# Performance work log

Measured on AMD Instinct MI355X. Metric: run time of the kernel, lower is better.

The kernel has to match this reference:

```python
import jax, jax.numpy as jnp
import numpy as np

N_NODES = 100000
N_EDGES = 1200000
IN_DIM = 256
HID = 64


def _spmm(rows, cols, vals, M):
    # sparse (COO) @ dense: gather source rows, scale by edge vals, scatter-add to dest
    gathered = M[cols] * vals[:, None]          # [E, d]
    return jax.ops.segment_sum(gathered, rows, num_segments=N_NODES)


def _gcn_embed(rows, cols, vals, X, W1, b1, W2, b2):
    # layer 1: SELU(A @ (X W1) + b1)
    Z = _spmm(rows, cols, vals, X @ W1) + b1
    Z = jax.nn.selu(Z)
    # layer 2: A @ (Z W2) + b2 (no activation)
    Z = _spmm(rows, cols, vals, Z @ W2) + b2
    # row-wise L2 normalize (F.normalize, p=2, dim=1)
    norm = jnp.sqrt(jnp.sum(Z * Z, axis=1, keepdims=True))
    return Z / jnp.maximum(norm, 1e-12)


def setup_inputs() -> dict:
    key = jax.random.key(0)
    ks = jax.random.split(key, 10)
    X1 = jax.random.normal(ks[0], (N_NODES, IN_DIM), dtype=jnp.float32)
    X2 = jax.random.normal(ks[1], (N_NODES, IN_DIM), dtype=jnp.float32)
    rows1 = jax.random.randint(ks[2], (N_EDGES,), 0, N_NODES, dtype=jnp.int32)
    cols1 = jax.random.randint(ks[3], (N_EDGES,), 0, N_NODES, dtype=jnp.int32)
    vals1 = jax.random.uniform(ks[4], (N_EDGES,), dtype=jnp.float32)
    rows2 = jax.random.randint(ks[5], (N_EDGES,), 0, N_NODES, dtype=jnp.int32)
    cols2 = jax.random.randint(ks[6], (N_EDGES,), 0, N_NODES, dtype=jnp.int32)
    vals2 = jax.random.uniform(ks[7], (N_EDGES,), dtype=jnp.float32)
    # Xavier-uniform weights, zero biases (reset_parameters)
    lim1 = float(np.sqrt(6.0 / (IN_DIM + HID)))
    lim2 = float(np.sqrt(6.0 / (HID + HID)))
    W1 = jax.random.uniform(ks[8], (IN_DIM, HID), dtype=jnp.float32, minval=-lim1, maxval=lim1)
    W2 = jax.random.uniform(ks[9], (HID, HID), dtype=jnp.float32, minval=-lim2, maxval=lim2)
    b1 = jnp.zeros((HID,), dtype=jnp.float32)
    b2 = jnp.zeros((HID,), dtype=jnp.float32)
    return {"X1": X1, "X2": X2, "rows1": rows1, "cols1": cols1, "vals1": vals1,
            "rows2": rows2, "cols2": cols2, "vals2": vals2,
            "W1": W1, "b1": b1, "W2": W2, "b2": b2}


def reference(X1, X2, rows1, cols1, vals1, rows2, cols2, vals2, W1, b1, W2, b2):
    Z1 = _gcn_embed(rows1, cols1, vals1, X1, W1, b1, W2, b2)
    Z2 = _gcn_embed(rows2, cols2, vals2, X2, W1, b1, W2, b2)
    return (Z1, Z2)
```

## Files before the change

### kernel.cpp

```cpp
#include <hip/hip_runtime.h>
#include <hip/hip_bf16.h>


#define RPB 512
#define EPB 4096
#define MAXB 8192

typedef __attribute__((ext_vector_type(8))) short short8;
typedef __attribute__((ext_vector_type(4))) short short4v;
typedef __attribute__((ext_vector_type(4))) float f32x4;

#define GEMM_LDS 36864
#define SCAT_LDS 52224
#define SORT_LDS 72704

__device__ __forceinline__ float selu_f(float x) {
    const float scale = 1.0507009873554805f;
    const float alpha = 1.6732632423543772f;
    return x > 0.0f ? scale * x : scale * alpha * (__expf(x) - 1.0f);
}

__device__ __forceinline__ short f2bf(float x) {
    unsigned u = __float_as_uint(x);
    u += 0x7FFF + ((u >> 16) & 1);
    return (short)(u >> 16);
}
__device__ __forceinline__ float bf2f(short h) {
    return __uint_as_float(((unsigned)(unsigned short)h) << 16);
}

__global__ void scan_a(const int* __restrict__ countsB, int* __restrict__ offsB,
                       int* __restrict__ partialsB, int N) {
    const int* counts = countsB + (size_t)blockIdx.y * N;
    int* offs = offsB + (size_t)blockIdx.y * (N + 1);
    int* partials = partialsB + (size_t)blockIdx.y * 512;
    __shared__ int sh[256];
    int tid = threadIdx.x;
    int base = blockIdx.x * 1024 + tid * 4;
    int4 c = make_int4(0, 0, 0, 0);
    if (base + 3 < N) {
        c = *(const int4*)(counts + base);
    } else {
        if (base + 0 < N) c.x = counts[base + 0];
        if (base + 1 < N) c.y = counts[base + 1];
        if (base + 2 < N) c.z = counts[base + 2];
        if (base + 3 < N) c.w = counts[base + 3];
    }
    int tsum = c.x + c.y + c.z + c.w;
    sh[tid] = tsum;
    __syncthreads();
    int val = tsum;
    for (int d = 1; d < 256; d <<= 1) {
        int t = (tid >= d) ? sh[tid - d] : 0;
        __syncthreads();
        val += t;
        sh[tid] = val;
        __syncthreads();
    }
    int excl = val - tsum;
    int4 o;
    o.x = excl; o.y = o.x + c.x; o.z = o.y + c.y; o.w = o.z + c.z;
    if (base + 3 < N) {
        *(int4*)(offs + base) = o;
    } else {
        if (base + 0 < N) offs[base + 0] = o.x;
        if (base + 1 < N) offs[base + 1] = o.y;
        if (base + 2 < N) offs[base + 2] = o.z;
        if (base + 3 < N) offs[base + 3] = o.w;
    }
    if (tid == 255) partials[blockIdx.x] = val;
}

__global__ void scan_b(int* __restrict__ partialsB, int nb) {
    int* partials = partialsB + (size_t)blockIdx.y * 512;
    __shared__ int sh[128];
    int tid = threadIdx.x;
    int v = (tid < nb) ? partials[tid] : 0;
    sh[tid] = v;
    __syncthreads();
    int val = v;
    for (int d = 1; d < 128; d <<= 1) {
        int t = (tid >= d) ? sh[tid - d] : 0;
        __syncthreads();
        val += t;
        sh[tid] = val;
        __syncthreads();
    }
    if (tid < nb) partials[tid] = val - v;
}

__global__ void scan_c(int* __restrict__ offsB, const int* __restrict__ partialsB,
                       int N, int E) {
    int* offs = offsB + (size_t)blockIdx.y * (N + 1);
    const int* partials = partialsB + (size_t)blockIdx.y * 512;
    int tid = threadIdx.x;
    int base = blockIdx.x * 1024 + tid * 4;
    int add = partials[blockIdx.x];
    if (base + 3 < N) {
        int4 o = *(int4*)(offs + base);
        o.x += add; o.y += add; o.z += add; o.w += add;
        *(int4*)(offs + base) = o;
    } else {
        for (int t = 0; t < 4; t++)
            if (base + t < N) offs[base + t] += add;
    }
    if (blockIdx.x == 0 && tid == 0) offs[N] = E;
}


__device__ __forceinline__ void role_hist(const int* __restrict__ rows,
                                          int* __restrict__ cntT,
                                          int E, int nbA, int NB, int bx,
                                          int* cnt) {
    int tid = threadIdx.x;
    cnt[tid] = 0;
    __syncthreads();
    int e0 = bx * EPB;
#pragma unroll
    for (int k = 0; k < EPB / 256; k++) {
        int e = e0 + k * 256 + tid;
        if (e < E) atomicAdd(&cnt[rows[e] >> 9], 1);
    }
    __syncthreads();
    if (tid < NB) cntT[tid * nbA + bx] = cnt[tid];
}

__device__ __forceinline__ void role_scatter(const int* __restrict__ rows,
                                             const int* __restrict__ cols,
                                             const float* __restrict__ vals,
                                             const int* __restrict__ csOffs,
                                             int2* __restrict__ ecvA,
                                             int E, int nbA, int NB, int bx,
                                             char* smem) {
    int* cnt = (int*)smem;
    int* loc = cnt + 256;
    int* gof = loc + 256;
    int* dstBase = gof + 256;
    int2* eLDS = (int2*)(dstBase + EPB);
    int tid = threadIdx.x;
    int e0 = bx * EPB;
    cnt[tid] = 0;
    __syncthreads();
#pragma unroll
    for (int k = 0; k < EPB / 256; k++) {
        int e = e0 + k * 256 + tid;
        if (e < E) atomicAdd(&cnt[rows[e] >> 9], 1);
    }
    __syncthreads();
    int my = cnt[tid];
    loc[tid] = my;
    __syncthreads();
    int val = my;
    for (int d = 1; d < 256; d <<= 1) {
        int t = (tid >= d) ? loc[tid - d] : 0;
        __syncthreads();
        val += t;
        loc[tid] = val;
        __syncthreads();
    }
    int excl = val - my;
    loc[tid] = excl;
    cnt[tid] = excl;
    gof[tid] = (tid < NB) ? csOffs[tid * nbA + bx] : 0;
    __syncthreads();
#pragma unroll
    for (int k = 0; k < EPB / 256; k++) {
        int e = e0 + k * 256 + tid;
        if (e < E) {
            int r = rows[e];
            int b = r >> 9;
            int p = atomicAdd(&cnt[b], 1);
            eLDS[p] = make_int2(((r & (RPB - 1)) << 17) | cols[e],
                                __float_as_int(vals[e]));
            dstBase[p] = gof[b] - loc[b];
        }
    }
    __syncthreads();
    int nE = min(EPB, E - e0);
    for (int j = tid; j < nE; j += 256)
        ecvA[dstBase[j] + j] = eLDS[j];
}

__device__ __forceinline__ void role_sort(const int* __restrict__ csOffs,
                                          const int2* __restrict__ ecvA,
                                          int2* __restrict__ ecv,
                                          int* __restrict__ offs,
                                          int nbA, int N, int E, int b,
                                          char* smem) {
    int* rcnt = (int*)smem;
    int* roff = rcnt + 512;
    int* rcur = roff + 512;
    int* sh   = rcur + 512;
    int2* eLDS = (int2*)(sh + 256);
    int tid = threadIdx.x;
    int bs = csOffs[b * nbA];
    int be = csOffs[(b + 1) * nbA];
    int cntE = be - bs;
    if (cntE > MAXB) cntE = MAXB;
    rcnt[tid] = 0;
    rcnt[tid + 256] = 0;
    __syncthreads();
    for (int j = tid; j < cntE; j += 256)
        atomicAdd(&rcnt[ecvA[bs + j].x >> 17], 1);
    __syncthreads();
    int a0 = rcnt[2 * tid], a1 = rcnt[2 * tid + 1];
    int ps = a0 + a1;
    sh[tid] = ps;
    __syncthreads();
    int val = ps;
    for (int d = 1; d < 256; d <<= 1) {
        int t = (tid >= d) ? sh[tid - d] : 0;
        __syncthreads();
        val += t;
        sh[tid] = val;
        __syncthreads();
    }
    int exclPair = val - ps;
    roff[2 * tid] = exclPair;
    roff[2 * tid + 1] = exclPair + a0;
    rcur[2 * tid] = exclPair;
    rcur[2 * tid + 1] = exclPair + a0;
    __syncthreads();
    int row0 = b * RPB;
    for (int t2 = tid; t2 < RPB; t2 += 256) {
        int row = row0 + t2;
        if (row <= N) offs[row] = bs + roff[t2];
    }
    if (b == 0 && tid == 0) offs[N] = E;
    for (int j = tid; j < cntE; j += 256) {
        int2 p = ecvA[bs + j];
        int pos = atomicAdd(&rcur[p.x >> 17], 1);
        if (pos < MAXB) eLDS[pos] = make_int2(p.x & 0x1FFFF, p.y);
    }
    __syncthreads();
    for (int j = tid; j < cntE; j += 256)
        ecv[bs + j] = eLDS[j];
}

__device__ __forceinline__ void role_gemm256(const float* __restrict__ A,
                                             const short* __restrict__ Wth,
                                             const short* __restrict__ Wtl,
                                             float* __restrict__ C, int M,
                                             int tile, char* smem) {
    constexpr int K = 256, NC = K / 64;
    short* Ah = (short*)smem;
    short* Al = Ah + 64 * 72;
    short* Wh = Al + 64 * 72;
    short* Wl = Wh + 64 * 72;
    int tid = threadIdx.x;
    int wave = tid >> 6, lane = tid & 63;
    int m = lane & 15, q = lane >> 4;
    int row0 = tile * 64;
    int ai = tid >> 4;
    int aj = (tid & 15) * 4;
    f32x4 acc[4] = {{0.f, 0.f, 0.f, 0.f}, {0.f, 0.f, 0.f, 0.f},
                    {0.f, 0.f, 0.f, 0.f}, {0.f, 0.f, 0.f, 0.f}};
    float4 ga[4];
#pragma unroll
    for (int v = 0; v < 4; v++) {
        int gr = row0 + v * 16 + ai;
        ga[v] = make_float4(0.f, 0.f, 0.f, 0.f);
        if (gr < M) ga[v] = *(const float4*)(A + (size_t)gr * K + aj);
    }
#pragma unroll
    for (int c = 0; c < NC; c++) {
        short4v whv[4], wlv[4];
#pragma unroll
        for (int v = 0; v < 4; v++) {
            size_t wo = (size_t)(v * 16 + ai) * K + c * 64 + aj;
            whv[v] = *(const short4v*)(Wth + wo);
            wlv[v] = *(const short4v*)(Wtl + wo);
        }
        float4 gan[4];
        if (c + 1 < NC) {
#pragma unroll
            for (int v = 0; v < 4; v++) {
                int gr = row0 + v * 16 + ai;
                gan[v] = make_float4(0.f, 0.f, 0.f, 0.f);
                if (gr < M)
                    gan[v] = *(const float4*)(A + (size_t)gr * K + (c + 1) * 64 + aj);
            }
        }
#pragma unroll
        for (int v = 0; v < 4; v++) {
            int r = v * 16 + ai;
            float f[4] = {ga[v].x, ga[v].y, ga[v].z, ga[v].w};
            short4v h, l;
#pragma unroll
            for (int j = 0; j < 4; j++) {
                short hh = f2bf(f[j]);
                h[j] = hh;
                l[j] = f2bf(f[j] - bf2f(hh));
            }
            *(short4v*)(&Ah[r * 72 + aj]) = h;
            *(short4v*)(&Al[r * 72 + aj]) = l;
        }
#pragma unroll
        for (int v = 0; v < 4; v++) {
            int n = v * 16 + ai;
            *(short4v*)(&Wh[n * 72 + aj]) = whv[v];
            *(short4v*)(&Wl[n * 72 + aj]) = wlv[v];
        }
        __syncthreads();
        int ar = (16 * wave + m) * 72;
        short8 ah0 = *(const short8*)(&Ah[ar + q * 8]);
        short8 ah1 = *(const short8*)(&Ah[ar + 32 + q * 8]);
        short8 al0 = *(const short8*)(&Al[ar + q * 8]);
        short8 al1 = *(const short8*)(&Al[ar + 32 + q * 8]);
#pragma unroll
        for (int nt = 0; nt < 4; nt++) {
            int nb = (nt * 16 + m) * 72;
            short8 bh0 = *(const short8*)(&Wh[nb + q * 8]);
            short8 bh1 = *(const short8*)(&Wh[nb + 32 + q * 8]);
            short8 bl0 = *(const short8*)(&Wl[nb + q * 8]);
            short8 bl1 = *(const short8*)(&Wl[nb + 32 + q * 8]);
            acc[nt] = __builtin_amdgcn_mfma_f32_16x16x32_bf16(ah0, bh0, acc[nt], 0, 0, 0);
            acc[nt] = __builtin_amdgcn_mfma_f32_16x16x32_bf16(al0, bh0, acc[nt], 0, 0, 0);
            acc[nt] = __builtin_amdgcn_mfma_f32_16x16x32_bf16(ah0, bl0, acc[nt], 0, 0, 0);
            acc[nt] = __builtin_amdgcn_mfma_f32_16x16x32_bf16(ah1, bh1, acc[nt], 0, 0, 0);
            acc[nt] = __builtin_amdgcn_mfma_f32_16x16x32_bf16(al1, bh1, acc[nt], 0, 0, 0);
            acc[nt] = __builtin_amdgcn_mfma_f32_16x16x32_bf16(ah1, bl1, acc[nt], 0, 0, 0);
        }
        if (c + 1 < NC) {
            __syncthreads();
#pragma unroll
            for (int v = 0; v < 4; v++) ga[v] = gan[v];
        }
    }
#pragma unroll
    for (int nt = 0; nt < 4; nt++) {
#pragma unroll
        for (int r = 0; r < 4; r++) {
            int grow = row0 + 16 * wave + q * 4 + r;
            if (grow < M) C[(size_t)grow * 64 + nt * 16 + m] = acc[nt][r];
        }
    }
}


__global__ __launch_bounds__(256) void fat_hist_gemm(
        const int* __restrict__ r0, const int* __restrict__ r1,
        int* __restrict__ cntTB, int E, int nbA, int NB, int Mcnt,
        const float* __restrict__ X1, const float* __restrict__ X2,
        const short* __restrict__ w1th, const short* __restrict__ w1tl,
        float* __restrict__ C0, float* __restrict__ C1, int Nn,
        int t0, int tcnt) {
    __shared__ __align__(16) char smem[GEMM_LDS];
    int id = blockIdx.x;
    int nCsr = 2 * nbA;
    if (id < nCsr) {
        int gph = id / nbA, bx = id % nbA;
        role_hist(gph ? r1 : r0, cntTB + (size_t)gph * Mcnt, E, nbA, NB, bx,
                  (int*)smem);
    } else {
        int gid = id - nCsr;
        int gph = gid / tcnt;
        int tile = t0 + gid - gph * tcnt;
        role_gemm256(gph ? X2 : X1, w1th, w1tl, gph ? C1 : C0, Nn, tile, smem);
    }
}

__global__ __launch_bounds__(256) void fat_scatter_gemm(
        const int* __restrict__ r0, const int* __restrict__ r1,
        const int* __restrict__ c0, const int* __restrict__ c1,
        const float* __restrict__ v0, const float* __restrict__ v1,
        const int* __restrict__ csOffsB, int2* __restrict__ ecvAB,
        int E, int nbA, int NB, int Mcnt,
        const float* __restrict__ X1, const float* __restrict__ X2,
        const short* __restrict__ w1th, const short* __restrict__ w1tl,
        float* __restrict__ C0, float* __restrict__ C1, int Nn,
        int t0, int tcnt) {
    __shared__ __align__(16) char smem[SCAT_LDS];
    int id = blockIdx.x;
    int nCsr = 2 * nbA;
    if (id < nCsr) {
        int gph = id / nbA, bx = id % nbA;
        role_scatter(gph ? r1 : r0, gph ? c1 : c0, gph ? v1 : v0,
                     csOffsB + (size_t)gph * (Mcnt + 1),
                     ecvAB + (size_t)gph * E, E, nbA, NB, bx, smem);
    } else {
        int gid = id - nCsr;
        int gph = gid / tcnt;
        int tile = t0 + gid - gph * tcnt;
        role_gemm256(gph ? X2 : X1, w1th, w1tl, gph ? C1 : C0, Nn, tile, smem);
    }
}

__global__ __launch_bounds__(256) void fat_sort_gemm(
        const int* __restrict__ csOffsB, const int2* __restrict__ ecvAB,
        int2* __restrict__ ecvB, int* __restrict__ offsB,
        int nbA, int N, int E, int Mcnt, int NB,
        const float* __restrict__ X1, const float* __restrict__ X2,
        const short* __restrict__ w1th, const short* __restrict__ w1tl,
        float* __restrict__ C0, float* __restrict__ C1, int Nn,
        int t0, int tcnt) {
    __shared__ __align__(16) char smem[SORT_LDS];
    int id = blockIdx.x;
    int nCsr = 2 * NB;
    if (id < nCsr) {
        int gph = id / NB, b = id % NB;
        role_sort(csOffsB + (size_t)gph * (Mcnt + 1),
                  ecvAB + (size_t)gph * E,
                  ecvB + (size_t)gph * E,
                  offsB + (size_t)gph * (N + 1),
                  nbA, N, E, b, smem);
    } else {
        int gid = id - nCsr;
        int gph = gid / tcnt;
        int tile = t0 + gid - gph * tcnt;
        role_gemm256(gph ? X2 : X1, w1th, w1tl, gph ? C1 : C0, Nn, tile, smem);
    }
}

__global__ void prep_w2(const float* __restrict__ W1, short* __restrict__ th1,
                        short* __restrict__ tl1,
                        const float* __restrict__ W2, short* __restrict__ th2,
                        short* __restrict__ tl2) {
    int idx = blockIdx.x * 256 + threadIdx.x;
    const int n1 = 256 * 64;
    if (idx < n1) {
        int k = idx >> 6, n = idx & 63;
        float x = W1[idx];
        short h = f2bf(x);
        short l = f2bf(x - bf2f(h));
        th1[n * 256 + k] = h;
        tl1[n * 256 + k] = l;
    } else if (idx - n1 < 64 * 64) {
        int i2 = idx - n1;
        int k = i2 >> 6, n = i2 & 63;
        float x = W2[i2];
        short h = f2bf(x);
        short l = f2bf(x - bf2f(h));
        th2[n * 64 + k] = h;
        tl2[n * 64 + k] = l;
    }
}

__device__ __forceinline__ void spmm_row4(const int* __restrict__ offs,
                                          const int2* __restrict__ ecv,
                                          const float* __restrict__ H,
                                          int row, int g, int f4,
                                          float& ax, float& ay, float& az, float& aw) {
    int s = offs[row], e = offs[row + 1];
    s = __builtin_amdgcn_readfirstlane(s);
    e = __builtin_amdgcn_readfirstlane(e);
    ax = ay = az = aw = 0.f;
    for (int i = s; i < e; i += 16) {
        int i0 = i + g, i1 = i + 4 + g, i2 = i + 8 + g, i3 = i + 12 + g;
        int2 p0 = ecv[i0 < e ? i0 : (e - 1)];
        int2 p1 = ecv[i1 < e ? i1 : (e - 1)];
        int2 p2 = ecv[i2 < e ? i2 : (e - 1)];
        int2 p3 = ecv[i3 < e ? i3 : (e - 1)];
        float v0 = (i0 < e) ? __int_as_float(p0.y) : 0.f;
        float v1 = (i1 < e) ? __int_as_float(p1.y) : 0.f;
        float v2 = (i2 < e) ? __int_as_float(p2.y) : 0.f;
        float v3 = (i3 < e) ? __int_as_float(p3.y) : 0.f;
        float4 h0 = *(const float4*)(H + (size_t)p0.x * 64 + f4);
        float4 h1 = *(const float4*)(H + (size_t)p1.x * 64 + f4);
        float4 h2 = *(const float4*)(H + (size_t)p2.x * 64 + f4);
        float4 h3 = *(const float4*)(H + (size_t)p3.x * 64 + f4);
        ax = fmaf(v0, h0.x, ax); ay = fmaf(v0, h0.y, ay);
        az = fmaf(v0, h0.z, az); aw = fmaf(v0, h0.w, aw);
        ax = fmaf(v1, h1.x, ax); ay = fmaf(v1, h1.y, ay);
        az = fmaf(v1, h1.z, az); aw = fmaf(v1, h1.w, aw);
        ax = fmaf(v2, h2.x, ax); ay = fmaf(v2, h2.y, ay);
        az = fmaf(v2, h2.z, az); aw = fmaf(v2, h2.w, aw);
        ax = fmaf(v3, h3.x, ax); ay = fmaf(v3, h3.y, ay);
        az = fmaf(v3, h3.z, az); aw = fmaf(v3, h3.w, aw);
    }
#pragma unroll
    for (int d = 16; d <= 32; d <<= 1) {
        ax += __shfl_xor(ax, d, 64);
        ay += __shfl_xor(ay, d, 64);
        az += __shfl_xor(az, d, 64);
        aw += __shfl_xor(aw, d, 64);
    }
}

__global__ __launch_bounds__(256) void spmm_selu_w2(const int* __restrict__ offsB,
                                                    const int2* __restrict__ ecvB,
                                                    const float* __restrict__ HB,
                                                    const float* __restrict__ bias,
                                                    const short* __restrict__ w2th,
                                                    const short* __restrict__ w2tl,
                                                    float* __restrict__ outB,
                                                    int N, int E) {
    int gph = blockIdx.y;
    const int* offs = offsB + (size_t)gph * (N + 1);
    const int2* ecv = ecvB + (size_t)gph * E;
    const float* H = HB + (size_t)gph * N * 64;
    float* out = outB + (size_t)gph * N * 64;
    __shared__ short Zh[16 * 72], Zl[16 * 72];
    int tid = threadIdx.x, wave = tid >> 6, lane = tid & 63;
    int g = lane >> 4, f4 = (lane & 15) * 4;
    int rbase = blockIdx.x * 16;
    float4 b = *(const float4*)(bias + f4);
#pragma unroll
    for (int rr = 0; rr < 4; rr++) {
        int lr = wave * 4 + rr;
        int row = rbase + lr;
        if (row < N) {
            float ax, ay, az, aw;
            spmm_row4(offs, ecv, H, row, g, f4, ax, ay, az, aw);
            if (g == 0) {
                float zx = selu_f(ax + b.x);
                float zy = selu_f(ay + b.y);
                float zz = selu_f(az + b.z);
                float zw = selu_f(aw + b.w);
                short4v h, l;
                h.x = f2bf(zx); l.x = f2bf(zx - bf2f(h.x));
                h.y = f2bf(zy); l.y = f2bf(zy - bf2f(h.y));
                h.z = f2bf(zz); l.z = f2bf(zz - bf2f(h.z));
                h.w = f2bf(zw); l.w = f2bf(zw - bf2f(h.w));
                *(short4v*)(&Zh[lr * 72 + f4]) = h;
                *(short4v*)(&Zl[lr * 72 + f4]) = l;
            }
        } else if (g == 0) {
            short4v zv = {0, 0, 0, 0};
            *(short4v*)(&Zh[lr * 72 + f4]) = zv;
            *(short4v*)(&Zl[lr * 72 + f4]) = zv;
        }
    }
    __syncthreads();
    int m_ = lane & 15, q = lane >> 4;
    int ar = m_ * 72;
    short8 ah0 = *(const short8*)(&Zh[ar + q * 8]);
    short8 ah1 = *(const short8*)(&Zh[ar + 32 + q * 8]);
    short8 al0 = *(const short8*)(&Zl[ar + q * 8]);
    short8 al1 = *(const short8*)(&Zl[ar + 32 + q * 8]);
    const short* bhp = w2th + (size_t)(wave * 16 + m_) * 64;
    const short* blp = w2tl + (size_t)(wave * 16 + m_) * 64;
    short8 bh0 = *(const short8*)(bhp + q * 8);
    short8 bh1 = *(const short8*)(bhp + 32 + q * 8);
    short8 bl0 = *(const short8*)(blp + q * 8);
    short8 bl1 = *(const short8*)(blp + 32 + q * 8);
    f32x4 acc = {0.f, 0.f, 0.f, 0.f};
    acc = __builtin_amdgcn_mfma_f32_16x16x32_bf16(ah0, bh0, acc, 0, 0, 0);
    acc = __builtin_amdgcn_mfma_f32_16x16x32_bf16(al0, bh0, acc, 0, 0, 0);
    acc = __builtin_amdgcn_mfma_f32_16x16x32_bf16(ah0, bl0, acc, 0, 0, 0);
    acc = __builtin_amdgcn_mfma_f32_16x16x32_bf16(ah1, bh1, acc, 0, 0, 0);
    acc = __builtin_amdgcn_mfma_f32_16x16x32_bf16(al1, bh1, acc, 0, 0, 0);
    acc = __builtin_amdgcn_mfma_f32_16x16x32_bf16(ah1, bl1, acc, 0, 0, 0);
#pragma unroll
    for (int r = 0; r < 4; r++) {
        int grow = rbase + q * 4 + r;
        if (grow < N) out[(size_t)grow * 64 + wave * 16 + m_] = acc[r];
    }
}

__global__ __launch_bounds__(256) void spmm_norm(const int* __restrict__ offsB,
                                                 const int2* __restrict__ ecvB,
                                                 const float* __restrict__ HB,
                                                 const float* __restrict__ bias,
                                                 float* __restrict__ outB,
                                                 int N, int E) {
    int gph = blockIdx.y;
    const int* offs = offsB + (size_t)gph * (N + 1);
    const int2* ecv = ecvB + (size_t)gph * E;
    const float* H = HB + (size_t)gph * N * 64;
    float* out = outB + (size_t)gph * N * 64;
    int row = blockIdx.x * 4 + (threadIdx.x >> 6);
    if (row >= N) return;
    int lane = threadIdx.x & 63;
    int g = lane >> 4, f4 = (lane & 15) * 4;
    float ax, ay, az, aw;
    spmm_row4(offs, ecv, H, row, g, f4, ax, ay, az, aw);
    float4 b = *(const float4*)(bias + f4);
    float zx = ax + b.x, zy = ay + b.y, zz = az + b.z, zw = aw + b.w;
    float s2 = zx * zx + zy * zy + zz * zz + zw * zw;
#pragma unroll
    for (int d = 1; d <= 8; d <<= 1) s2 += __shfl_xor(s2, d, 64);
    float inv = 1.0f / fmaxf(sqrtf(s2), 1e-12f);
    if (g == 0) {
        float4 o;
        o.x = zx * inv; o.y = zy * inv; o.z = zz * inv; o.w = zw * inv;
        *(float4*)(out + (size_t)row * 64 + f4) = o;
    }
}

extern "C" void kernel_launch(void* const* d_in, const int* in_sizes, int n_in,
                              void* d_out, int out_size, void* d_ws, size_t ws_size,
                              hipStream_t stream) {
    const int IN_DIM = 256, HID = 64;
    const int N = in_sizes[0] / IN_DIM;
    const int E = in_sizes[2];

    const float* X1 = (const float*)d_in[0];
    const float* X2 = (const float*)d_in[1];
    const int*   r0 = (const int*)d_in[2];
    const int*   c0 = (const int*)d_in[3];
    const float* v0 = (const float*)d_in[4];
    const int*   r1 = (const int*)d_in[5];
    const int*   c1 = (const int*)d_in[6];
    const float* v1 = (const float*)d_in[7];
    const float* W1 = (const float*)d_in[8];
    const float* b1 = (const float*)d_in[9];
    const float* W2 = (const float*)d_in[10];
    const float* b2 = (const float*)d_in[11];
    float* out = (float*)d_out;

    const int NB  = (N + RPB - 1) / RPB;
    const int nbA = (E + EPB - 1) / EPB;
    const int M   = NB * nbA;
    const int nbScanM = (M + 1023) / 1024;
    const int nbGemm = (N + 63) / 64;
    const int nbRow  = (N + 3) / 4;
    const int nbFuse = (N + 15) / 16;

    const int T1 = nbGemm / 10;
    const int T2 = (nbGemm * 45) / 100;
    const int T3 = nbGemm - T1 - T2;

    auto align16 = [](char* p) { return (char*)(((uintptr_t)p + 15) & ~(uintptr_t)15); };
    char* w = (char*)d_ws;
    float* bufA   = (float*)w; w += (size_t)2 * N * HID * sizeof(float);
    float* bufB   = (float*)w; w += (size_t)2 * N * HID * sizeof(float);
    w = align16(w);
    int2*  ecv    = (int2*)w;  w += (size_t)2 * E * sizeof(int2);
    w = align16(w);
    int2*  ecvA   = (int2*)w;  w += (size_t)2 * E * sizeof(int2);
    w = align16(w);
    int*   cntT   = (int*)w;   w += (size_t)2 * M * sizeof(int);
    w = align16(w);
    int*   csOffs = (int*)w;   w += (size_t)2 * (M + 1) * sizeof(int);
    w = align16(w);
    int*   offs   = (int*)w;   w += (size_t)2 * (N + 1) * sizeof(int);
    w = align16(w);
    int*   partials = (int*)w; w += 2 * 512 * sizeof(int);
    w = align16(w);
    short* w1th = (short*)w;   w += (size_t)64 * IN_DIM * sizeof(short);
    short* w1tl = (short*)w;   w += (size_t)64 * IN_DIM * sizeof(short);
    short* w2th = (short*)w;   w += (size_t)64 * HID * sizeof(short);
    short* w2tl = (short*)w;   w += (size_t)64 * HID * sizeof(short);
    float* bufA1 = bufA + (size_t)N * HID;

    prep_w2<<<(IN_DIM * 64 + HID * 64 + 255) / 256, 256, 0, stream>>>(
        W1, w1th, w1tl, W2, w2th, w2tl);

    fat_hist_gemm<<<2 * nbA + 2 * T1, 256, 0, stream>>>(
        r0, r1, cntT, E, nbA, NB, M,
        X1, X2, w1th, w1tl, bufA, bufA1, N, 0, T1);
    scan_a<<<dim3(nbScanM, 2), 256, 0, stream>>>(cntT, csOffs, partials, M);
    scan_b<<<dim3(1, 2), 128, 0, stream>>>(partials, nbScanM);
    scan_c<<<dim3(nbScanM, 2), 256, 0, stream>>>(csOffs, partials, M, E);
    fat_scatter_gemm<<<2 * nbA + 2 * T2, 256, 0, stream>>>(
        r0, r1, c0, c1, v0, v1, csOffs, ecvA, E, nbA, NB, M,
        X1, X2, w1th, w1tl, bufA, bufA1, N, T1, T2);
    fat_sort_gemm<<<2 * NB + 2 * T3, 256, 0, stream>>>(
        csOffs, ecvA, ecv, offs, nbA, N, E, M, NB,
        X1, X2, w1th, w1tl, bufA, bufA1, N, T1 + T2, T3);

    spmm_selu_w2<<<dim3(nbFuse, 2), 256, 0, stream>>>(offs, ecv, bufA, b1,
                                                      w2th, w2tl, bufB, N, E);
    spmm_norm<<<dim3(nbRow, 2), 256, 0, stream>>>(offs, ecv, bufB, b2, out, N, E);
}
```

Before: 504.5 us.

## Stagger graph layers across kernels, read W1 directly, rebalance GEMM split

The layer-2 SpMM stages are restructured so that graph 0's layer-2 norm pass runs in the same kernel as graph 1's layer-1 SELU/W2 pass. Blocks interleave the two roles, one SELU block per four norm blocks, to overlap different work mixes and cut a kernel boundary's tail. The GEMM role now loads W1 hi/lo fragments straight from global memory, not staging them through LDS. This halves GEMM LDS use, which may raise occupancy, at the cost of more global/L2 reads. The GEMM tile split across the hist, scatter and sort kernels changes from proportional fractions to fixed caps of 300 and 750 tiles.

```diff
diff --git a/kernel.cpp b/kernel.cpp
--- a/kernel.cpp
+++ b/kernel.cpp
@@ -10,7 +10,7 @@
 typedef __attribute__((ext_vector_type(4))) short short4v;
 typedef __attribute__((ext_vector_type(4))) float f32x4;
 
-#define GEMM_LDS 36864
+#define GEMM_LDS 18432
 #define SCAT_LDS 52224
 #define SORT_LDS 72704
 
@@ -245,8 +245,6 @@
     constexpr int K = 256, NC = K / 64;
     short* Ah = (short*)smem;
     short* Al = Ah + 64 * 72;
-    short* Wh = Al + 64 * 72;
-    short* Wl = Wh + 64 * 72;
     int tid = threadIdx.x;
     int wave = tid >> 6, lane = tid & 63;
     int m = lane & 15, q = lane >> 4;
@@ -264,13 +262,6 @@
     }
 #pragma unroll
     for (int c = 0; c < NC; c++) {
-        short4v whv[4], wlv[4];
-#pragma unroll
-        for (int v = 0; v < 4; v++) {
-            size_t wo = (size_t)(v * 16 + ai) * K + c * 64 + aj;
-            whv[v] = *(const short4v*)(Wth + wo);
-            wlv[v] = *(const short4v*)(Wtl + wo);
-        }
         float4 gan[4];
         if (c + 1 < NC) {
 #pragma unroll
@@ -295,12 +286,6 @@
             *(short4v*)(&Ah[r * 72 + aj]) = h;
             *(short4v*)(&Al[r * 72 + aj]) = l;
         }
-#pragma unroll
-        for (int v = 0; v < 4; v++) {
-            int n = v * 16 + ai;
-            *(short4v*)(&Wh[n * 72 + aj]) = whv[v];
-            *(short4v*)(&Wl[n * 72 + aj]) = wlv[v];
-        }
         __syncthreads();
         int ar = (16 * wave + m) * 72;
         short8 ah0 = *(const short8*)(&Ah[ar + q * 8]);
@@ -309,11 +294,12 @@
         short8 al1 = *(const short8*)(&Al[ar + 32 + q * 8]);
 #pragma unroll
         for (int nt = 0; nt < 4; nt++) {
-            int nb = (nt * 16 + m) * 72;
-            short8 bh0 = *(const short8*)(&Wh[nb + q * 8]);
-            short8 bh1 = *(const short8*)(&Wh[nb + 32 + q * 8]);
-            short8 bl0 = *(const short8*)(&Wl[nb + q * 8]);
-            short8 bl1 = *(const short8*)(&Wl[nb + 32 + q * 8]);
+            const short* bhp = Wth + (size_t)(nt * 16 + m) * K + c * 64;
+            const short* blp = Wtl + (size_t)(nt * 16 + m) * K + c * 64;
+            short8 bh0 = *(const short8*)(bhp + q * 8);
+            short8 bh1 = *(const short8*)(bhp + 32 + q * 8);
+            short8 bl0 = *(const short8*)(blp + q * 8);
+            short8 bl1 = *(const short8*)(blp + 32 + q * 8);
             acc[nt] = __builtin_amdgcn_mfma_f32_16x16x32_bf16(ah0, bh0, acc[nt], 0, 0, 0);
             acc[nt] = __builtin_amdgcn_mfma_f32_16x16x32_bf16(al0, bh0, acc[nt], 0, 0, 0);
             acc[nt] = __builtin_amdgcn_mfma_f32_16x16x32_bf16(ah0, bl0, acc[nt], 0, 0, 0);
@@ -334,105 +320,6 @@
             int grow = row0 + 16 * wave + q * 4 + r;
             if (grow < M) C[(size_t)grow * 64 + nt * 16 + m] = acc[nt][r];
         }
-    }
-}
-
-
-__global__ __launch_bounds__(256) void fat_hist_gemm(
-        const int* __restrict__ r0, const int* __restrict__ r1,
-        int* __restrict__ cntTB, int E, int nbA, int NB, int Mcnt,
-        const float* __restrict__ X1, const float* __restrict__ X2,
-        const short* __restrict__ w1th, const short* __restrict__ w1tl,
-        float* __restrict__ C0, float* __restrict__ C1, int Nn,
-        int t0, int tcnt) {
-    __shared__ __align__(16) char smem[GEMM_LDS];
-    int id = blockIdx.x;
-    int nCsr = 2 * nbA;
-    if (id < nCsr) {
-        int gph = id / nbA, bx = id % nbA;
-        role_hist(gph ? r1 : r0, cntTB + (size_t)gph * Mcnt, E, nbA, NB, bx,
-                  (int*)smem);
-    } else {
-        int gid = id - nCsr;
-        int gph = gid / tcnt;
-        int tile = t0 + gid - gph * tcnt;
-        role_gemm256(gph ? X2 : X1, w1th, w1tl, gph ? C1 : C0, Nn, tile, smem);
-    }
-}
-
-__global__ __launch_bounds__(256) void fat_scatter_gemm(
-        const int* __restrict__ r0, const int* __restrict__ r1,
-        const int* __restrict__ c0, const int* __restrict__ c1,
-        const float* __restrict__ v0, const float* __restrict__ v1,
-        const int* __restrict__ csOffsB, int2* __restrict__ ecvAB,
-        int E, int nbA, int NB, int Mcnt,
-        const float* __restrict__ X1, const float* __restrict__ X2,
-        const short* __restrict__ w1th, const short* __restrict__ w1tl,
-        float* __restrict__ C0, float* __restrict__ C1, int Nn,
-        int t0, int tcnt) {
-    __shared__ __align__(16) char smem[SCAT_LDS];
-    int id = blockIdx.x;
-    int nCsr = 2 * nbA;
-    if (id < nCsr) {
-        int gph = id / nbA, bx = id % nbA;
-        role_scatter(gph ? r1 : r0, gph ? c1 : c0, gph ? v1 : v0,
-                     csOffsB + (size_t)gph * (Mcnt + 1),
-                     ecvAB + (size_t)gph * E, E, nbA, NB, bx, smem);
-    } else {
-        int gid = id - nCsr;
-        int gph = gid / tcnt;
-        int tile = t0 + gid - gph * tcnt;
-        role_gemm256(gph ? X2 : X1, w1th, w1tl, gph ? C1 : C0, Nn, tile, smem);
-    }
-}
-
-__global__ __launch_bounds__(256) void fat_sort_gemm(
-        const int* __restrict__ csOffsB, const int2* __restrict__ ecvAB,
-        int2* __restrict__ ecvB, int* __restrict__ offsB,
-        int nbA, int N, int E, int Mcnt, int NB,
-        const float* __restrict__ X1, const float* __restrict__ X2,
-        const short* __restrict__ w1th, const short* __restrict__ w1tl,
-        float* __restrict__ C0, float* __restrict__ C1, int Nn,
-        int t0, int tcnt) {
-    __shared__ __align__(16) char smem[SORT_LDS];
-    int id = blockIdx.x;
-    int nCsr = 2 * NB;
-    if (id < nCsr) {
-        int gph = id / NB, b = id % NB;
-        role_sort(csOffsB + (size_t)gph * (Mcnt + 1),
-                  ecvAB + (size_t)gph * E,
-                  ecvB + (size_t)gph * E,
-                  offsB + (size_t)gph * (N + 1),
-                  nbA, N, E, b, smem);
-    } else {
-        int gid = id - nCsr;
-        int gph = gid / tcnt;
-        int tile = t0 + gid - gph * tcnt;
-        role_gemm256(gph ? X2 : X1, w1th, w1tl, gph ? C1 : C0, Nn, tile, smem);
-    }
-}
-
-__global__ void prep_w2(const float* __restrict__ W1, short* __restrict__ th1,
-                        short* __restrict__ tl1,
-                        const float* __restrict__ W2, short* __restrict__ th2,
-                        short* __restrict__ tl2) {
-    int idx = blockIdx.x * 256 + threadIdx.x;
-    const int n1 = 256 * 64;
-    if (idx < n1) {
-        int k = idx >> 6, n = idx & 63;
-        float x = W1[idx];
-        short h = f2bf(x);
-        short l = f2bf(x - bf2f(h));
-        th1[n * 256 + k] = h;
-        tl1[n * 256 + k] = l;
-    } else if (idx - n1 < 64 * 64) {
-        int i2 = idx - n1;
-        int k = i2 >> 6, n = i2 & 63;
-        float x = W2[i2];
-        short h = f2bf(x);
-        short l = f2bf(x - bf2f(h));
-        th2[n * 64 + k] = h;
-        tl2[n * 64 + k] = l;
     }
 }
 
@@ -477,23 +364,19 @@
     }
 }
 
-__global__ __launch_bounds__(256) void spmm_selu_w2(const int* __restrict__ offsB,
-                                                    const int2* __restrict__ ecvB,
-                                                    const float* __restrict__ HB,
-                                                    const float* __restrict__ bias,
-                                                    const short* __restrict__ w2th,
-                                                    const short* __restrict__ w2tl,
-                                                    float* __restrict__ outB,
-                                                    int N, int E) {
-    int gph = blockIdx.y;
-    const int* offs = offsB + (size_t)gph * (N + 1);
-    const int2* ecv = ecvB + (size_t)gph * E;
-    const float* H = HB + (size_t)gph * N * 64;
-    float* out = outB + (size_t)gph * N * 64;
-    __shared__ short Zh[16 * 72], Zl[16 * 72];
+__device__ __forceinline__ void role_selu(const int* __restrict__ offs,
+                                          const int2* __restrict__ ecv,
+                                          const float* __restrict__ H,
+                                          const float* __restrict__ bias,
+                                          const short* __restrict__ w2th,
+                                          const short* __restrict__ w2tl,
+                                          float* __restrict__ out,
+                                          int N, int bx, char* smemc) {
+    short* Zh = (short*)smemc;
+    short* Zl = Zh + 16 * 72;
     int tid = threadIdx.x, wave = tid >> 6, lane = tid & 63;
     int g = lane >> 4, f4 = (lane & 15) * 4;
-    int rbase = blockIdx.x * 16;
+    int rbase = bx * 16;
     float4 b = *(const float4*)(bias + f4);
 #pragma unroll
     for (int rr = 0; rr < 4; rr++) {
@@ -548,18 +431,13 @@
     }
 }
 
-__global__ __launch_bounds__(256) void spmm_norm(const int* __restrict__ offsB,
-                                                 const int2* __restrict__ ecvB,
-                                                 const float* __restrict__ HB,
-                                                 const float* __restrict__ bias,
-                                                 float* __restrict__ outB,
-                                                 int N, int E) {
-    int gph = blockIdx.y;
-    const int* offs = offsB + (size_t)gph * (N + 1);
-    const int2* ecv = ecvB + (size_t)gph * E;
-    const float* H = HB + (size_t)gph * N * 64;
-    float* out = outB + (size_t)gph * N * 64;
-    int row = blockIdx.x * 4 + (threadIdx.x >> 6);
+__device__ __forceinline__ void role_norm(const int* __restrict__ offs,
+                                          const int2* __restrict__ ecv,
+                                          const float* __restrict__ H,
+                                          const float* __restrict__ bias,
+                                          float* __restrict__ out,
+                                          int N, int bx) {
+    int row = bx * 4 + (threadIdx.x >> 6);
     if (row >= N) return;
     int lane = threadIdx.x & 63;
     int g = lane >> 4, f4 = (lane & 15) * 4;
@@ -575,6 +453,138 @@
         float4 o;
         o.x = zx * inv; o.y = zy * inv; o.z = zz * inv; o.w = zw * inv;
         *(float4*)(out + (size_t)row * 64 + f4) = o;
+    }
+}
+
+
+__global__ __launch_bounds__(256) void fat_hist_gemm(
+        const int* __restrict__ r0, const int* __restrict__ r1,
+        int* __restrict__ cntTB, int E, int nbA, int NB, int Mcnt,
+        const float* __restrict__ X1, const float* __restrict__ X2,
+        const short* __restrict__ w1th, const short* __restrict__ w1tl,
+        float* __restrict__ C0, float* __restrict__ C1, int Nn,
+        int t0, int tcnt) {
+    __shared__ __align__(16) char smem[GEMM_LDS];
+    int id = blockIdx.x;
+    int nCsr = 2 * nbA;
+    if (id < nCsr) {
+        int gph = id / nbA, bx = id % nbA;
+        role_hist(gph ? r1 : r0, cntTB + (size_t)gph * Mcnt, E, nbA, NB, bx,
+                  (int*)smem);
+    } else {
+        int gid = id - nCsr;
+        int gph = gid / tcnt;
+        int tile = t0 + gid - gph * tcnt;
+        role_gemm256(gph ? X2 : X1, w1th, w1tl, gph ? C1 : C0, Nn, tile, smem);
+    }
+}
+
+__global__ __launch_bounds__(256) void fat_scatter_gemm(
+        const int* __restrict__ r0, const int* __restrict__ r1,
+        const int* __restrict__ c0, const int* __restrict__ c1,
+        const float* __restrict__ v0, const float* __restrict__ v1,
+        const int* __restrict__ csOffsB, int2* __restrict__ ecvAB,
+        int E, int nbA, int NB, int Mcnt,
+        const float* __restrict__ X1, const float* __restrict__ X2,
+        const short* __restrict__ w1th, const short* __restrict__ w1tl,
+        float* __restrict__ C0, float* __restrict__ C1, int Nn,
+        int t0, int tcnt) {
+    __shared__ __align__(16) char smem[SCAT_LDS];
+    int id = blockIdx.x;
+    int nCsr = 2 * nbA;
+    if (id < nCsr) {
+        int gph = id / nbA, bx = id % nbA;
+        role_scatter(gph ? r1 : r0, gph ? c1 : c0, gph ? v1 : v0,
+                     csOffsB + (size_t)gph * (Mcnt + 1),
+                     ecvAB + (size_t)gph * E, E, nbA, NB, bx, smem);
+    } else {
+        int gid = id - nCsr;
+        int gph = gid / tcnt;
+        int tile = t0 + gid - gph * tcnt;
+        role_gemm256(gph ? X2 : X1, w1th, w1tl, gph ? C1 : C0, Nn, tile, smem);
+    }
+}
+
+__global__ __launch_bounds__(256) void fat_sort_gemm(
+        const int* __restrict__ csOffsB, const int2* __restrict__ ecvAB,
+        int2* __restrict__ ecvB, int* __restrict__ offsB,
+        int nbA, int N, int E, int Mcnt, int NB,
+        const float* __restrict__ X1, const float* __restrict__ X2,
+        const short* __restrict__ w1th, const short* __restrict__ w1tl,
+        float* __restrict__ C0, float* __restrict__ C1, int Nn,
+        int t0, int tcnt) {
+    __shared__ __align__(16) char smem[SORT_LDS];
+    int id = blockIdx.x;
+    int nCsr = 2 * NB;
+    if (id < nCsr) {
+        int gph = id / NB, b = id % NB;
+        role_sort(csOffsB + (size_t)gph * (Mcnt + 1),
+                  ecvAB + (size_t)gph * E,
+                  ecvB + (size_t)gph * E,
+                  offsB + (size_t)gph * (N + 1),
+                  nbA, N, E, b, smem);
+    } else {
+        int gid = id - nCsr;
+        int gph = gid / tcnt;
+        int tile = t0 + gid - gph * tcnt;
+        role_gemm256(gph ? X2 : X1, w1th, w1tl, gph ? C1 : C0, Nn, tile, smem);
+    }
+}
+
+__global__ __launch_bounds__(256) void spmm_selu_one(
+        const int* __restrict__ offs, const int2* __restrict__ ecv,
+        const float* __restrict__ H, const float* __restrict__ bias,
+        const short* __restrict__ w2th, const short* __restrict__ w2tl,
+        float* __restrict__ out, int N) {
+    __shared__ __align__(16) char smem[4608];
+    role_selu(offs, ecv, H, bias, w2th, w2tl, out, N, blockIdx.x, smem);
+}
+
+__global__ __launch_bounds__(256) void fat_norm_selu(
+        const int* __restrict__ offs0, const int2* __restrict__ ecv0,
+        const float* __restrict__ Y0, const float* __restrict__ b2_,
+        float* __restrict__ out0,
+        const int* __restrict__ offs1, const int2* __restrict__ ecv1,
+        const float* __restrict__ H1, const float* __restrict__ b1_,
+        const short* __restrict__ w2th, const short* __restrict__ w2tl,
+        float* __restrict__ Y1, int N) {
+    __shared__ __align__(16) char smem[4608];
+    int id = blockIdx.x;
+    int j = id / 5, r = id - j * 5;
+    if (r == 0)
+        role_selu(offs1, ecv1, H1, b1_, w2th, w2tl, Y1, N, j, smem);
+    else
+        role_norm(offs0, ecv0, Y0, b2_, out0, N, j * 4 + r - 1);
+}
+
+__global__ __launch_bounds__(256) void spmm_norm_one(
+        const int* __restrict__ offs, const int2* __restrict__ ecv,
+        const float* __restrict__ H, const float* __restrict__ bias,
+        float* __restrict__ out, int N) {
+    role_norm(offs, ecv, H, bias, out, N, blockIdx.x);
+}
+
+__global__ void prep_w2(const float* __restrict__ W1, short* __restrict__ th1,
+                        short* __restrict__ tl1,
+                        const float* __restrict__ W2, short* __restrict__ th2,
+                        short* __restrict__ tl2) {
+    int idx = blockIdx.x * 256 + threadIdx.x;
+    const int n1 = 256 * 64;
+    if (idx < n1) {
+        int k = idx >> 6, n = idx & 63;
+        float x = W1[idx];
+        short h = f2bf(x);
+        short l = f2bf(x - bf2f(h));
+        th1[n * 256 + k] = h;
+        tl1[n * 256 + k] = l;
+    } else if (idx - n1 < 64 * 64) {
+        int i2 = idx - n1;
+        int k = i2 >> 6, n = i2 & 63;
+        float x = W2[i2];
+        short h = f2bf(x);
+        short l = f2bf(x - bf2f(h));
+        th2[n * 64 + k] = h;
+        tl2[n * 64 + k] = l;
     }
 }
 
@@ -604,12 +614,11 @@
     const int M   = NB * nbA;
     const int nbScanM = (M + 1023) / 1024;
     const int nbGemm = (N + 63) / 64;
-    const int nbRow  = (N + 3) / 4;
     const int nbFuse = (N + 15) / 16;
 
-    const int T1 = nbGemm / 10;
-    const int T2 = (nbGemm * 45) / 100;
-    const int T3 = nbGemm - T1 - T2;
+    int Th  = nbGemm < 300 ? nbGemm : 300;
+    int Tsc = (nbGemm - Th) < 750 ? (nbGemm - Th) : 750;
+    int Tsr = nbGemm - Th - Tsc;
 
     auto align16 = [](char* p) { return (char*)(((uintptr_t)p + 15) & ~(uintptr_t)15); };
     char* w = (char*)d_ws;
@@ -633,24 +642,31 @@
     short* w2th = (short*)w;   w += (size_t)64 * HID * sizeof(short);
     short* w2tl = (short*)w;   w += (size_t)64 * HID * sizeof(short);
     float* bufA1 = bufA + (size_t)N * HID;
+    float* bufB1 = bufB + (size_t)N * HID;
+    const int* offs1p = offs + (N + 1);
+    int2* ecv1p = ecv + (size_t)E;
 
     prep_w2<<<(IN_DIM * 64 + HID * 64 + 255) / 256, 256, 0, stream>>>(
         W1, w1th, w1tl, W2, w2th, w2tl);
 
-    fat_hist_gemm<<<2 * nbA + 2 * T1, 256, 0, stream>>>(
+    fat_hist_gemm<<<2 * nbA + 2 * Th, 256, 0, stream>>>(
         r0, r1, cntT, E, nbA, NB, M,
-        X1, X2, w1th, w1tl, bufA, bufA1, N, 0, T1);
+        X1, X2, w1th, w1tl, bufA, bufA1, N, 0, Th);
     scan_a<<<dim3(nbScanM, 2), 256, 0, stream>>>(cntT, csOffs, partials, M);
     scan_b<<<dim3(1, 2), 128, 0, stream>>>(partials, nbScanM);
     scan_c<<<dim3(nbScanM, 2), 256, 0, stream>>>(csOffs, partials, M, E);
-    fat_scatter_gemm<<<2 * nbA + 2 * T2, 256, 0, stream>>>(
+    fat_scatter_gemm<<<2 * nbA + 2 * Tsc, 256, 0, stream>>>(
         r0, r1, c0, c1, v0, v1, csOffs, ecvA, E, nbA, NB, M,
-        X1, X2, w1th, w1tl, bufA, bufA1, N, T1, T2);
-    fat_sort_gemm<<<2 * NB + 2 * T3, 256, 0, stream>>>(
+        X1, X2, w1th, w1tl, bufA, bufA1, N, Th, Tsc);
+    fat_sort_gemm<<<2 * NB + 2 * Tsr, 256, 0, stream>>>(
         csOffs, ecvA, ecv, offs, nbA, N, E, M, NB,
-        X1, X2, w1th, w1tl, bufA, bufA1, N, T1 + T2, T3);
-
-    spmm_selu_w2<<<dim3(nbFuse, 2), 256, 0, stream>>>(offs, ecv, bufA, b1,
-                                                      w2th, w2tl, bufB, N, E);
-    spmm_norm<<<dim3(nbRow, 2), 256, 0, stream>>>(offs, ecv, bufB, b2, out, N, E);
-}
+        X1, X2, w1th, w1tl, bufA, bufA1, N, Th + Tsc, Tsr);
+
+    spmm_selu_one<<<nbFuse, 256, 0, stream>>>(offs, ecv, bufA, b1,
+                                              w2th, w2tl, bufB, N);
+    fat_norm_selu<<<5 * nbFuse, 256, 0, stream>>>(
+        offs, ecv, bufB, b2, out,
+        offs1p, ecv1p, bufA1, b1, w2th, w2tl, bufB1, N);
+    spmm_norm_one<<<4 * nbFuse, 256, 0, stream>>>(
+        offs1p, ecv1p, bufB1, b2, out + (size_t)N * HID, N);
+}
```

New measurement: 590.2 us. 1.17x slower.
